# Performance work log

Measured on AMD Instinct MI355X. Metric: run time of the kernel, lower is better.

Reference implementation:

```python
import jax, jax.numpy as jnp
import numpy as np

N = 16384
IN = 64
H = 128
OUT = 64
K = 32


def setup_inputs() -> dict:
    key = jax.random.key(0)
    ks = jax.random.split(key, 5)

    def unif(k, shape):
        fan_in = shape[1]
        std = 1.0 / np.sqrt(fan_in)
        return jax.random.uniform(k, shape, jnp.float32, -std, std)

    x = jax.random.normal(ks[0], (N, IN), jnp.float32)
    w0 = unif(ks[1], (H, 2 * IN))            # layer 0: in_dim = 64
    w2_0 = unif(ks[2], (OUT, IN + H))
    in1 = IN + OUT                            # dense concat: 128
    w1 = unif(ks[3], (H, 2 * in1))
    w2_1 = unif(ks[4], (OUT, in1 + H))
    return {"x": x, "w0": w0, "w2_0": w2_0, "w1": w1, "w2_1": w2_1}


def _affinity_kernel(x, w, w2, k):
    # kNN graph via squared Euclidean distances (monotone in torch.norm)
    sq = jnp.sum(x * x, axis=1)
    d2 = sq[:, None] + sq[None, :] - 2.0 * (x @ x.T)   # (N, N)
    _, idx = jax.lax.top_k(-d2, k)                      # k smallest distances, (N, k)
    nbr = x[idx]                                        # (N, k, D) gather
    self_b = jnp.broadcast_to(x[:, None, :], nbr.shape)
    cat = jnp.concatenate([nbr, self_b], axis=-1)       # (N, k, 2D)
    h = jnp.einsum('nkd,hd->nkh', cat, w)
    h = jnp.clip(h, -1.0, 1.0)                          # Hardtanh
    pooled = h.mean(axis=1)                             # average pooling, (N, H)
    return jnp.concatenate([pooled, x], axis=-1) @ w2.T  # (N, out_dim)


def reference(x, w0, w2_0, w1, w2_1):
    o0 = _affinity_kernel(x, w0, w2_0, K)
    x1 = jnp.concatenate([x, o0], axis=-1)   # dense connectivity (forward_input=True)
    o1 = _affinity_kernel(x1, w1, w2_1, K)
    return o1
```

## Files before the change

### kernel.cpp

```cpp
#include <hip/hip_runtime.h>
#include <hip/hip_bf16.h>

#define NP   16384
#define KNN  32
#define HDIM 128
#define ODIM 64

typedef __attribute__((ext_vector_type(8))) short bf16x8;
typedef __attribute__((ext_vector_type(4))) float f32x4;

__global__ __launch_bounds__(256)
void split_kernel(const float* __restrict__ X, unsigned short* __restrict__ hi,
                  unsigned short* __restrict__ lo, int n4) {
    const int i = blockIdx.x * 256 + threadIdx.x;
    if (i >= n4) return;
    const float4 v = reinterpret_cast<const float4*>(X)[i];
    const float vv[4] = {v.x, v.y, v.z, v.w};
    ushort4 h, l;
    unsigned short* hp = &h.x;
    unsigned short* lp = &l.x;
    #pragma unroll
    for (int c = 0; c < 4; ++c) {
        __hip_bfloat16 hb = __float2bfloat16(vv[c]);
        const float hf = __bfloat162float(hb);
        __hip_bfloat16 lb = __float2bfloat16(vv[c] - hf);
        hp[c] = *reinterpret_cast<unsigned short*>(&hb);
        lp[c] = *reinterpret_cast<unsigned short*>(&lb);
    }
    reinterpret_cast<ushort4*>(hi)[i] = h;
    reinterpret_cast<ushort4*>(lo)[i] = l;
}

template<int D>
__global__ __launch_bounds__(256)
void sq_kernel(const float* __restrict__ X, float* __restrict__ sq) {
    const int lane = threadIdx.x & 63;
    const int row  = blockIdx.x * 4 + (threadIdx.x >> 6);
    float s = 0.f;
    #pragma unroll
    for (int d = lane; d < D; d += 64) {
        const float v = X[(size_t)row * D + d];
        s = fmaf(v, v, s);
    }
    #pragma unroll
    for (int off = 32; off; off >>= 1) s += __shfl_down(s, off);
    if (lane == 0) sq[row] = s;
}

template<int D>
__global__ __launch_bounds__(512, 4)
void topk_kernel(const unsigned short* __restrict__ Xhi,
                 const unsigned short* __restrict__ Xlo,
                 const float* __restrict__ sq, int* __restrict__ topIdx) {
    constexpr int TI = 16, JC = 128, SS = JC + 1;
    constexpr int NT = NP / JC;
    constexpr int KQ = D / 8;
    constexpr int KS = D / 32;
    constexpr int PLSLOT = JC * KQ;
    constexpr int CALLS = 2 * PLSLOT / 512;
    __shared__ __align__(16) unsigned short xjB[2 * PLSLOT * 8];
    __shared__ float scoresR[TI * SS];

    const int t = threadIdx.x;
    const int lane = t & 63;
    const int waveU = __builtin_amdgcn_readfirstlane(t >> 6);
    const int rowBase = blockIdx.x * TI;
    const int l15 = lane & 15, l4 = lane >> 4;
    const float INF = __builtin_inff();
    const int jcol = 16 * waveU + l15;

    bf16x8 Ahi[KS], Alo[KS];
    #pragma unroll
    for (int s = 0; s < KS; ++s) {
        const size_t off = (size_t)(rowBase + l15) * D + 32 * s + 8 * l4;
        Ahi[s] = *reinterpret_cast<const bf16x8*>(Xhi + off);
        Alo[s] = *reinterpret_cast<const bf16x8*>(Xlo + off);
    }

    float tv[2]; int tidx[2]; float minv[2];
    #pragma unroll
    for (int r = 0; r < 2; ++r) { tv[r] = -INF; tidx[r] = 0x7fffffff; minv[r] = -INF; }

    auto stageTile = [&](int jb) {
        #pragma unroll
        for (int c = 0; c < CALLS; ++c) {
            const int slotBase = (waveU * CALLS + c) * 64;
            const int sl = slotBase + lane;
            const int pl = sl / PLSLOT;
            const int ps = sl % PLSLOT;
            const int j  = ps / KQ;
            const int kq = (ps % KQ) ^ (j & (KQ - 1));
            const unsigned short* src =
                (pl ? Xlo : Xhi) + (size_t)(jb + j) * D + 8 * kq;
            __builtin_amdgcn_global_load_lds(
                (const __attribute__((address_space(1))) void*)src,
                (__attribute__((address_space(3))) void*)&xjB[(size_t)slotBase * 8],
                16, 0, 0);
        }
    };

    stageTile(0);
    __syncthreads();

    for (int it = 0; it < NT; ++it) {
        const int jb = it * JC;
        const float sub0 = 0.5f * sq[jb + lane];
        const float sub1 = 0.5f * sq[jb + 64 + lane];

        f32x4 Ca = {0,0,0,0}, Cb = {0,0,0,0}, Cc = {0,0,0,0};
        #pragma unroll
        for (int s = 0; s < KS; ++s) {
            const int kq = 4 * s + l4;
            const int slot = jcol * KQ + (kq ^ (jcol & (KQ - 1)));
            const bf16x8 Bh = *reinterpret_cast<const bf16x8*>(&xjB[(size_t)slot * 8]);
            const bf16x8 Bl = *reinterpret_cast<const bf16x8*>(&xjB[(size_t)(PLSLOT + slot) * 8]);
            Ca = __builtin_amdgcn_mfma_f32_16x16x32_bf16(Ahi[s], Bh, Ca, 0, 0, 0);
            Cb = __builtin_amdgcn_mfma_f32_16x16x32_bf16(Ahi[s], Bl, Cb, 0, 0, 0);
            Cc = __builtin_amdgcn_mfma_f32_16x16x32_bf16(Alo[s], Bh, Cc, 0, 0, 0);
        }
        #pragma unroll
        for (int r = 0; r < 4; ++r)
            scoresR[(4 * l4 + r) * SS + jcol] = (Ca[r] + Cb[r]) + Cc[r];
        __syncthreads();

        if (it + 1 < NT) stageTile(jb + JC);

        #pragma unroll
        for (int h = 0; h < 2; ++h) {
            float sv[2];
            unsigned long long m[2];
            #pragma unroll
            for (int r = 0; r < 2; ++r) {
                sv[r] = scoresR[(2 * waveU + r) * SS + h * 64 + lane]
                      - (h ? sub1 : sub0);
                m[r] = __ballot(sv[r] > minv[r]);
            }
            while (m[0] | m[1]) {
                #pragma unroll
                for (int r = 0; r < 2; ++r) {
                    if (m[r]) {
                        const int l = __builtin_ctzll(m[r]);
                        m[r] &= m[r] - 1;
                        const float cv = __shfl(sv[r], l);
                        const int   cj = jb + h * 64 + l;
                        const float upv = __shfl_up(tv[r], 1);
                        const int   upi = __shfl_up(tidx[r], 1);
                        const bool ge = (lane < KNN) && (tv[r] >= cv);
                        const int p = __popcll(__ballot(ge));
                        if (lane == p)                   { tv[r] = cv;  tidx[r] = cj; }
                        else if (lane > p && lane < KNN) { tv[r] = upv; tidx[r] = upi; }
                    }
                }
            }
        }
        #pragma unroll
        for (int r = 0; r < 2; ++r)
            minv[r] = __shfl(tv[r], KNN - 1);

        __syncthreads();
    }

    if (lane < KNN) {
        #pragma unroll
        for (int r = 0; r < 2; ++r)
            topIdx[(size_t)(rowBase + waveU * 2 + r) * KNN + lane] = tidx[r];
    }
}

template<int D, int LAYER>
__global__ __launch_bounds__(512)
void mlp_kernel(const float* __restrict__ X, const int* __restrict__ topIdx,
                const float* __restrict__ W, const float* __restrict__ W2,
                float* __restrict__ out) {
    constexpr int RPB = 2, WPR = 4, KPT = 8;
    constexpr int W2C  = HDIM + D;
    constexpr int SPL2 = 512 / (RPB * ODIM);
    constexpr int CL   = W2C / SPL2;
    __shared__ float AT[D * HDIM];
    __shared__ float nbrL[RPB][KNN][D];
    __shared__ float xi[RPB][D];
    __shared__ float part[RPB][WPR][HDIM];
    __shared__ int   idx_s[RPB][KNN];

    const int t = threadIdx.x;
    const int lane = t & 63;
    const int waveU = __builtin_amdgcn_readfirstlane(t >> 6);
    const int rowBase = blockIdx.x * RPB;
    const int row = waveU / WPR;
    const int wkb = waveU % WPR;
    const int hh2 = 2 * lane;

    if (t < RPB * D / 4) {
        const int i = t / (D / 4), dg = t % (D / 4);
        const float4 v = *reinterpret_cast<const float4*>(
            X + (size_t)(rowBase + i) * D + 4 * dg);
        xi[i][4 * dg + 0] = v.x; xi[i][4 * dg + 1] = v.y;
        xi[i][4 * dg + 2] = v.z; xi[i][4 * dg + 3] = v.w;
    }
    if (t < RPB * KNN)
        idx_s[t >> 5][t & 31] = topIdx[(size_t)(rowBase + (t >> 5)) * KNN + (t & 31)];
    for (int e = t; e < HDIM * D / 4; e += 512) {
        const int hh = e % HDIM, dg = e / HDIM;
        const float4 v = *reinterpret_cast<const float4*>(
            W + (size_t)hh * (2 * D) + D + 4 * dg);
        AT[(4 * dg + 0) * HDIM + hh] = v.x; AT[(4 * dg + 1) * HDIM + hh] = v.y;
        AT[(4 * dg + 2) * HDIM + hh] = v.z; AT[(4 * dg + 3) * HDIM + hh] = v.w;
    }
    __syncthreads();

    float hs0 = 0.f, hs1 = 0.f;
    #pragma unroll 8
    for (int d = 0; d < D; ++d) {
        const float a = xi[row][d];
        const float2 b = *reinterpret_cast<const float2*>(&AT[d * HDIM + hh2]);
        hs0 = fmaf(b.x, a, hs0);
        hs1 = fmaf(b.y, a, hs1);
    }
    __syncthreads();

    for (int e = t; e < HDIM * D / 4; e += 512) {
        const int hh = e % HDIM, dg = e / HDIM;
        const float4 v = *reinterpret_cast<const float4*>(
            W + (size_t)hh * (2 * D) + 4 * dg);
        AT[(4 * dg + 0) * HDIM + hh] = v.x; AT[(4 * dg + 1) * HDIM + hh] = v.y;
        AT[(4 * dg + 2) * HDIM + hh] = v.z; AT[(4 * dg + 3) * HDIM + hh] = v.w;
    }
    constexpr int G4 = RPB * KNN * D / 4;
    for (int e = t; e < G4; e += 512) {
        const int d4 = e % (D / 4);
        const int k  = (e / (D / 4)) % KNN;
        const int r  = e / (D / 4 * KNN);
        const float4 v = *reinterpret_cast<const float4*>(
            X + (size_t)idx_s[r][k] * D + 4 * d4);
        *reinterpret_cast<float4*>(&nbrL[r][k][4 * d4]) = v;
    }
    __syncthreads();

    float acc0[KPT], acc1[KPT];
    #pragma unroll
    for (int r = 0; r < KPT; ++r) { acc0[r] = 0.f; acc1[r] = 0.f; }

    for (int dg = 0; dg < D / 4; ++dg) {
        float4 b[KPT];
        #pragma unroll
        for (int r = 0; r < KPT; ++r)
            b[r] = *reinterpret_cast<const float4*>(&nbrL[row][wkb * KPT + r][4 * dg]);
        const float2 a0 = *reinterpret_cast<const float2*>(&AT[(4 * dg + 0) * HDIM + hh2]);
        const float2 a1 = *reinterpret_cast<const float2*>(&AT[(4 * dg + 1) * HDIM + hh2]);
        const float2 a2 = *reinterpret_cast<const float2*>(&AT[(4 * dg + 2) * HDIM + hh2]);
        const float2 a3 = *reinterpret_cast<const float2*>(&AT[(4 * dg + 3) * HDIM + hh2]);
        #pragma unroll
        for (int r = 0; r < KPT; ++r) {
            acc0[r] = fmaf(a0.x, b[r].x, acc0[r]); acc1[r] = fmaf(a0.y, b[r].x, acc1[r]);
            acc0[r] = fmaf(a1.x, b[r].y, acc0[r]); acc1[r] = fmaf(a1.y, b[r].y, acc1[r]);
            acc0[r] = fmaf(a2.x, b[r].z, acc0[r]); acc1[r] = fmaf(a2.y, b[r].z, acc1[r]);
            acc0[r] = fmaf(a3.x, b[r].w, acc0[r]); acc1[r] = fmaf(a3.y, b[r].w, acc1[r]);
        }
    }

    float p0 = 0.f, p1 = 0.f;
    #pragma unroll
    for (int r = 0; r < KPT; ++r) {
        p0 += fminf(1.f, fmaxf(-1.f, acc0[r] + hs0));
        p1 += fminf(1.f, fmaxf(-1.f, acc1[r] + hs1));
    }
    *reinterpret_cast<float2*>(&part[row][wkb][hh2]) =
        make_float2(p0 * (1.f / KNN), p1 * (1.f / KNN));
    __syncthreads();

    {
        const int og   = t / SPL2;
        const int spl  = t % SPL2;
        const int orow = og >> 6, o = og & 63;
        const int c0   = spl * CL;
        float s = 0.f;
        for (int c4 = 0; c4 < CL / 4; ++c4) {
            const int c = c0 + 4 * c4;
            const float4 w = *reinterpret_cast<const float4*>(W2 + (size_t)o * W2C + c);
            float vs[4];
            if (c < HDIM) {
                const float4 q0 = *reinterpret_cast<const float4*>(&part[orow][0][c]);
                const float4 q1 = *reinterpret_cast<const float4*>(&part[orow][1][c]);
                const float4 q2 = *reinterpret_cast<const float4*>(&part[orow][2][c]);
                const float4 q3 = *reinterpret_cast<const float4*>(&part[orow][3][c]);
                vs[0] = q0.x + q1.x + q2.x + q3.x;
                vs[1] = q0.y + q1.y + q2.y + q3.y;
                vs[2] = q0.z + q1.z + q2.z + q3.z;
                vs[3] = q0.w + q1.w + q2.w + q3.w;
            } else {
                const float4 xv = *reinterpret_cast<const float4*>(&xi[orow][c - HDIM]);
                vs[0] = xv.x; vs[1] = xv.y; vs[2] = xv.z; vs[3] = xv.w;
            }
            const float wv[4] = {w.x, w.y, w.z, w.w};
            #pragma unroll
            for (int j = 0; j < 4; ++j)
                s = fmaf(vs[j], wv[j], s);
        }
        #pragma unroll
        for (int off = SPL2 / 2; off; off >>= 1) s += __shfl_down(s, off);
        if (spl == 0) {
            if (LAYER == 0)
                out[(size_t)(rowBase + orow) * 128 + 64 + o] = s;
            else
                out[(size_t)(rowBase + orow) * ODIM + o] = s;
        }
    }
    if (LAYER == 0 && t < RPB * 64) {
        const int orow = t >> 6, d = t & 63;
        out[(size_t)(rowBase + orow) * 128 + d] = xi[orow][d];
    }
}

extern "C" void kernel_launch(void* const* d_in, const int* in_sizes, int n_in,
                              void* d_out, int out_size, void* d_ws, size_t ws_size,
                              hipStream_t stream) {
    const float* x    = (const float*)d_in[0];
    const float* w0   = (const float*)d_in[1];
    const float* w2_0 = (const float*)d_in[2];
    const float* w1   = (const float*)d_in[3];
    const float* w2_1 = (const float*)d_in[4];
    float* out = (float*)d_out;

    char* ws = (char*)d_ws;
    float* sq  = (float*)ws;
    int*   idx = (int*)(ws + (size_t)NP * 4);
    float* x1  = (float*)(ws + (size_t)NP * 4 + (size_t)NP * KNN * 4);
    unsigned short* xhi = (unsigned short*)(ws + (size_t)NP * 4
                          + (size_t)NP * KNN * 4 + (size_t)NP * HDIM * 4);
    unsigned short* xlo = xhi + (size_t)NP * HDIM;

    split_kernel<<<NP * 64 / 4 / 256, 256, 0, stream>>>(x, xhi, xlo, NP * 64 / 4);
    sq_kernel<64><<<NP / 4, 256, 0, stream>>>(x, sq);
    topk_kernel<64><<<NP / 16, 512, 0, stream>>>(xhi, xlo, sq, idx);
    mlp_kernel<64, 0><<<NP / 2, 512, 0, stream>>>(x, idx, w0, w2_0, x1);

    split_kernel<<<NP * 128 / 4 / 256, 256, 0, stream>>>(x1, xhi, xlo, NP * 128 / 4);
    sq_kernel<128><<<NP / 4, 256, 0, stream>>>(x1, sq);
    topk_kernel<128><<<NP / 16, 512, 0, stream>>>(xhi, xlo, sq, idx);
    mlp_kernel<128, 1><<<NP / 2, 512, 0, stream>>>(x1, idx, w1, w2_1, out);
}
```

Measured before the change: 2.126 ms.

## Compute neighbor-hidden projection in MLP kernel with split-bf16 MFMA

Replaces the FP32 FMA loop over gathered neighbors in the MLP kernel with bf16x3 split-precision MFMA (16x16x32). Neighbor rows are read directly from the existing hi/lo bf16 buffers instead of being gathered into shared memory. Pre-split weight halves are produced by a new small kernel. This removes the large nbrL shared buffer and the second weight transpose, cutting LDS use and ALU work. The cost is some precision loss from the 3-term bf16 emulation and added global gathers.

```diff
diff --git a/kernel.cpp b/kernel.cpp
--- a/kernel.cpp
+++ b/kernel.cpp
@@ -29,6 +29,20 @@
     }
     reinterpret_cast<ushort4*>(hi)[i] = h;
     reinterpret_cast<ushort4*>(lo)[i] = l;
+}
+
+__global__ __launch_bounds__(256)
+void wsplit_kernel(const float* __restrict__ W, unsigned short* __restrict__ hi,
+                   unsigned short* __restrict__ lo, int Dd) {
+    const int i = blockIdx.x * 256 + threadIdx.x;
+    if (i >= HDIM * Dd) return;
+    const int hh = i / Dd, d = i % Dd;
+    const float v = W[(size_t)hh * (2 * Dd) + d];
+    __hip_bfloat16 hb = __float2bfloat16(v);
+    const float hf = __bfloat162float(hb);
+    __hip_bfloat16 lb = __float2bfloat16(v - hf);
+    hi[i] = *reinterpret_cast<unsigned short*>(&hb);
+    lo[i] = *reinterpret_cast<unsigned short*>(&lb);
 }
 
 template<int D>
@@ -168,27 +182,30 @@
 }
 
 template<int D, int LAYER>
-__global__ __launch_bounds__(512)
-void mlp_kernel(const float* __restrict__ X, const int* __restrict__ topIdx,
+__global__ __launch_bounds__(512, 4)
+void mlp_kernel(const float* __restrict__ X,
+                const unsigned short* __restrict__ Xhi,
+                const unsigned short* __restrict__ Xlo,
+                const unsigned short* __restrict__ WAhi,
+                const unsigned short* __restrict__ WAlo,
                 const float* __restrict__ W, const float* __restrict__ W2,
-                float* __restrict__ out) {
-    constexpr int RPB = 2, WPR = 4, KPT = 8;
+                const int* __restrict__ topIdx, float* __restrict__ out) {
+    constexpr int RPB = 2;
+    constexpr int KS = D / 32;
     constexpr int W2C  = HDIM + D;
-    constexpr int SPL2 = 512 / (RPB * ODIM);
+    constexpr int SPL2 = 4;
     constexpr int CL   = W2C / SPL2;
     __shared__ float AT[D * HDIM];
-    __shared__ float nbrL[RPB][KNN][D];
     __shared__ float xi[RPB][D];
-    __shared__ float part[RPB][WPR][HDIM];
+    __shared__ float hself_s[RPB][HDIM];
+    __shared__ float part[RPB][2][HDIM];
     __shared__ int   idx_s[RPB][KNN];
 
     const int t = threadIdx.x;
     const int lane = t & 63;
     const int waveU = __builtin_amdgcn_readfirstlane(t >> 6);
     const int rowBase = blockIdx.x * RPB;
-    const int row = waveU / WPR;
-    const int wkb = waveU % WPR;
-    const int hh2 = 2 * lane;
+    const int l15 = lane & 15, l4 = lane >> 4;
 
     if (t < RPB * D / 4) {
         const int i = t / (D / 4), dg = t % (D / 4);
@@ -199,6 +216,13 @@
     }
     if (t < RPB * KNN)
         idx_s[t >> 5][t & 31] = topIdx[(size_t)(rowBase + (t >> 5)) * KNN + (t & 31)];
+    bf16x8 Ahi[KS], Alo[KS];
+    #pragma unroll
+    for (int s = 0; s < KS; ++s) {
+        const size_t off = (size_t)(waveU * 16 + l15) * D + 32 * s + 8 * l4;
+        Ahi[s] = *reinterpret_cast<const bf16x8*>(WAhi + off);
+        Alo[s] = *reinterpret_cast<const bf16x8*>(WAlo + off);
+    }
     for (int e = t; e < HDIM * D / 4; e += 512) {
         const int hh = e % HDIM, dg = e / HDIM;
         const float4 v = *reinterpret_cast<const float4*>(
@@ -208,64 +232,51 @@
     }
     __syncthreads();
 
-    float hs0 = 0.f, hs1 = 0.f;
-    #pragma unroll 8
-    for (int d = 0; d < D; ++d) {
-        const float a = xi[row][d];
-        const float2 b = *reinterpret_cast<const float2*>(&AT[d * HDIM + hh2]);
-        hs0 = fmaf(b.x, a, hs0);
-        hs1 = fmaf(b.y, a, hs1);
+    if (t < RPB * HDIM) {
+        const int row = t >> 7, hh = t & 127;
+        float s = 0.f;
+        #pragma unroll 8
+        for (int d = 0; d < D; ++d)
+            s = fmaf(AT[d * HDIM + hh], xi[row][d], s);
+        hself_s[row][hh] = s;
     }
     __syncthreads();
 
-    for (int e = t; e < HDIM * D / 4; e += 512) {
-        const int hh = e % HDIM, dg = e / HDIM;
-        const float4 v = *reinterpret_cast<const float4*>(
-            W + (size_t)hh * (2 * D) + 4 * dg);
-        AT[(4 * dg + 0) * HDIM + hh] = v.x; AT[(4 * dg + 1) * HDIM + hh] = v.y;
-        AT[(4 * dg + 2) * HDIM + hh] = v.z; AT[(4 * dg + 3) * HDIM + hh] = v.w;
-    }
-    constexpr int G4 = RPB * KNN * D / 4;
-    for (int e = t; e < G4; e += 512) {
-        const int d4 = e % (D / 4);
-        const int k  = (e / (D / 4)) % KNN;
-        const int r  = e / (D / 4 * KNN);
-        const float4 v = *reinterpret_cast<const float4*>(
-            X + (size_t)idx_s[r][k] * D + 4 * d4);
-        *reinterpret_cast<float4*>(&nbrL[r][k][4 * d4]) = v;
-    }
-    __syncthreads();
-
-    float acc0[KPT], acc1[KPT];
-    #pragma unroll
-    for (int r = 0; r < KPT; ++r) { acc0[r] = 0.f; acc1[r] = 0.f; }
-
-    for (int dg = 0; dg < D / 4; ++dg) {
-        float4 b[KPT];
-        #pragma unroll
-        for (int r = 0; r < KPT; ++r)
-            b[r] = *reinterpret_cast<const float4*>(&nbrL[row][wkb * KPT + r][4 * dg]);
-        const float2 a0 = *reinterpret_cast<const float2*>(&AT[(4 * dg + 0) * HDIM + hh2]);
-        const float2 a1 = *reinterpret_cast<const float2*>(&AT[(4 * dg + 1) * HDIM + hh2]);
-        const float2 a2 = *reinterpret_cast<const float2*>(&AT[(4 * dg + 2) * HDIM + hh2]);
-        const float2 a3 = *reinterpret_cast<const float2*>(&AT[(4 * dg + 3) * HDIM + hh2]);
-        #pragma unroll
-        for (int r = 0; r < KPT; ++r) {
-            acc0[r] = fmaf(a0.x, b[r].x, acc0[r]); acc1[r] = fmaf(a0.y, b[r].x, acc1[r]);
-            acc0[r] = fmaf(a1.x, b[r].y, acc0[r]); acc1[r] = fmaf(a1.y, b[r].y, acc1[r]);
-            acc0[r] = fmaf(a2.x, b[r].z, acc0[r]); acc1[r] = fmaf(a2.y, b[r].z, acc1[r]);
-            acc0[r] = fmaf(a3.x, b[r].w, acc0[r]); acc1[r] = fmaf(a3.y, b[r].w, acc1[r]);
-        }
-    }
-
-    float p0 = 0.f, p1 = 0.f;
-    #pragma unroll
-    for (int r = 0; r < KPT; ++r) {
-        p0 += fminf(1.f, fmaxf(-1.f, acc0[r] + hs0));
-        p1 += fminf(1.f, fmaxf(-1.f, acc1[r] + hs1));
-    }
-    *reinterpret_cast<float2*>(&part[row][wkb][hh2]) =
-        make_float2(p0 * (1.f / KNN), p1 * (1.f / KNN));
+    #pragma unroll
+    for (int a = 0; a < 4; ++a) {
+        const int row = a >> 1, kT = a & 1;
+        const int nIdx = idx_s[row][kT * 16 + l15];
+        bf16x8 Bh[KS], Bl[KS];
+        #pragma unroll
+        for (int s = 0; s < KS; ++s) {
+            const size_t off = (size_t)nIdx * D + 32 * s + 8 * l4;
+            Bh[s] = *reinterpret_cast<const bf16x8*>(Xhi + off);
+            Bl[s] = *reinterpret_cast<const bf16x8*>(Xlo + off);
+        }
+        f32x4 Ca = {0,0,0,0}, Cb = {0,0,0,0}, Cc = {0,0,0,0};
+        #pragma unroll
+        for (int s = 0; s < KS; ++s) {
+            Ca = __builtin_amdgcn_mfma_f32_16x16x32_bf16(Ahi[s], Bh[s], Ca, 0, 0, 0);
+            Cb = __builtin_amdgcn_mfma_f32_16x16x32_bf16(Ahi[s], Bl[s], Cb, 0, 0, 0);
+            Cc = __builtin_amdgcn_mfma_f32_16x16x32_bf16(Alo[s], Bh[s], Cc, 0, 0, 0);
+        }
+        float ps[4];
+        #pragma unroll
+        for (int r = 0; r < 4; ++r) {
+            const float h = (Ca[r] + Cb[r]) + Cc[r]
+                          + hself_s[row][waveU * 16 + 4 * l4 + r];
+            ps[r] = fminf(1.f, fmaxf(-1.f, h));
+        }
+        #pragma unroll
+        for (int off = 1; off <= 8; off <<= 1)
+            #pragma unroll
+            for (int r = 0; r < 4; ++r)
+                ps[r] += __shfl_xor(ps[r], off);
+        if (l15 == 0)
+            #pragma unroll
+            for (int r = 0; r < 4; ++r)
+                part[row][kT][waveU * 16 + 4 * l4 + r] = ps[r] * (1.f / KNN);
+    }
     __syncthreads();
 
     {
@@ -281,12 +292,8 @@
             if (c < HDIM) {
                 const float4 q0 = *reinterpret_cast<const float4*>(&part[orow][0][c]);
                 const float4 q1 = *reinterpret_cast<const float4*>(&part[orow][1][c]);
-                const float4 q2 = *reinterpret_cast<const float4*>(&part[orow][2][c]);
-                const float4 q3 = *reinterpret_cast<const float4*>(&part[orow][3][c]);
-                vs[0] = q0.x + q1.x + q2.x + q3.x;
-                vs[1] = q0.y + q1.y + q2.y + q3.y;
-                vs[2] = q0.z + q1.z + q2.z + q3.z;
-                vs[3] = q0.w + q1.w + q2.w + q3.w;
+                vs[0] = q0.x + q1.x; vs[1] = q0.y + q1.y;
+                vs[2] = q0.z + q1.z; vs[3] = q0.w + q1.w;
             } else {
                 const float4 xv = *reinterpret_cast<const float4*>(&xi[orow][c - HDIM]);
                 vs[0] = xv.x; vs[1] = xv.y; vs[2] = xv.z; vs[3] = xv.w;
@@ -328,14 +335,23 @@
     unsigned short* xhi = (unsigned short*)(ws + (size_t)NP * 4
                           + (size_t)NP * KNN * 4 + (size_t)NP * HDIM * 4);
     unsigned short* xlo = xhi + (size_t)NP * HDIM;
+    unsigned short* wa0hi = xlo + (size_t)NP * HDIM;
+    unsigned short* wa0lo = wa0hi + HDIM * 64;
+    unsigned short* wa1hi = wa0lo + HDIM * 64;
+    unsigned short* wa1lo = wa1hi + HDIM * 128;
+
+    wsplit_kernel<<<(HDIM * 64 + 255) / 256, 256, 0, stream>>>(w0, wa0hi, wa0lo, 64);
+    wsplit_kernel<<<(HDIM * 128 + 255) / 256, 256, 0, stream>>>(w1, wa1hi, wa1lo, 128);
 
     split_kernel<<<NP * 64 / 4 / 256, 256, 0, stream>>>(x, xhi, xlo, NP * 64 / 4);
     sq_kernel<64><<<NP / 4, 256, 0, stream>>>(x, sq);
     topk_kernel<64><<<NP / 16, 512, 0, stream>>>(xhi, xlo, sq, idx);
-    mlp_kernel<64, 0><<<NP / 2, 512, 0, stream>>>(x, idx, w0, w2_0, x1);
+    mlp_kernel<64, 0><<<NP / 2, 512, 0, stream>>>(x, xhi, xlo, wa0hi, wa0lo,
+                                                  w0, w2_0, idx, x1);
 
     split_kernel<<<NP * 128 / 4 / 256, 256, 0, stream>>>(x1, xhi, xlo, NP * 128 / 4);
     sq_kernel<128><<<NP / 4, 256, 0, stream>>>(x1, sq);
     topk_kernel<128><<<NP / 16, 512, 0, stream>>>(xhi, xlo, sq, idx);
-    mlp_kernel<128, 1><<<NP / 2, 512, 0, stream>>>(x1, idx, w1, w2_1, out);
-}
+    mlp_kernel<128, 1><<<NP / 2, 512, 0, stream>>>(x1, xhi, xlo, wa1hi, wa1lo,
+                                                   w1, w2_1, idx, out);
+}
```

Measured after the change: 1.972 ms. 1.08x faster.
